# Performance work log

Hardware: AMD Instinct MI355X
Metric: run time of the kernel (lower is better)

Reference implementation:

```python
import jax, jax.numpy as jnp
import numpy as np
from jax import lax

B, K, D = 8, 256, 256
T_FRAMES = 2048
NH, HD = 4, 64          # num_heads_upsampling = 2*num_heads, head_dim = in_dim // NH
FW = FC = 8             # filter_size_w / filter_size_c
SW, SC = 16, 2          # swish_block_units


def setup_inputs() -> dict:
    key = jax.random.key(0)
    ks = jax.random.split(key, 24)
    rn = lambda i, shape, s=0.05: jax.random.normal(ks[i], shape, jnp.float32) * s
    return {
        'phs': rn(0, (B, K, D), 1.0),
        'phs_mask': jnp.ones((B, K), bool),
        'total_duration_groundtruth': jnp.full((B,), T_FRAMES, jnp.int32),
        'T': T_FRAMES,
        'Wd': rn(1, (D, 1)), 'bd': jnp.zeros((1,), jnp.float32),
        'W1': rn(2, (D, D)), 'b1': jnp.zeros((D,), jnp.float32),
        'W2': rn(3, (D, D)), 'b2': jnp.zeros((D,), jnp.float32),
        'W3': rn(4, (D, D)), 'b3': jnp.zeros((D,), jnp.float32),
        'wconv_k': rn(5, (FW, D, 3)), 'wconv_b': jnp.zeros((FW,), jnp.float32),
        'wln_g': jnp.ones((FW,), jnp.float32), 'wln_b': jnp.zeros((FW,), jnp.float32),
        'cconv_k': rn(6, (FC, D, 3)), 'cconv_b': jnp.zeros((FC,), jnp.float32),
        'cln_g': jnp.ones((FC,), jnp.float32), 'cln_b': jnp.zeros((FC,), jnp.float32),
        'sw1_W': rn(7, (FW + 2, SW)), 'sw1_b': jnp.zeros((SW,), jnp.float32),
        'sw2_W': rn(8, (SW, SW)), 'sw2_b': jnp.zeros((SW,), jnp.float32),
        'sc1_W': rn(9, (FC + 2, SC)), 'sc1_b': jnp.zeros((SC,), jnp.float32),
        'sc2_W': rn(10, (SC, SC)), 'sc2_b': jnp.zeros((SC,), jnp.float32),
        'we_W': rn(11, (SW, NH)), 'we_b': jnp.zeros((NH,), jnp.float32),
        'ce_W': rn(12, (SC, HD)), 'ce_b': jnp.zeros((HD,), jnp.float32),
    }


def _silu(x):
    return x * jax.nn.sigmoid(x)


def _conv_ln_silu(x, kern, bias, g, beta):
    # x: (b,k,D) -> Conv1d (same pad) -> LayerNorm over channel dim -> SiLU -> (b,k,F)
    y = lax.conv_general_dilated(x.transpose(0, 2, 1), kern, (1,), [(1, 1)],
                                 dimension_numbers=('NCH', 'OIH', 'NCH'))
    y = y + bias[None, :, None]
    mu = y.mean(1, keepdims=True)
    var = y.var(1, keepdims=True)
    y = (y - mu) * lax.rsqrt(var + 1e-5) * g[None, :, None] + beta[None, :, None]
    return _silu(y).transpose(0, 2, 1)


def _forward(phs, phs_mask, total_duration_groundtruth, t,
             Wd, bd, W1, b1, W2, b2, W3, b3,
             wconv_k, wconv_b, wln_g, wln_b, cconv_k, cconv_b, cln_g, cln_b,
             sw1_W, sw1_b, sw2_W, sw2_b, sc1_W, sc1_b, sc2_W, sc2_b,
             we_W, we_b, ce_W, ce_b):
    b, k, D = phs.shape
    nh, hd = NH, HD
    v_pad = ~phs_mask                                       # (b,k)
    # duration predictor (encoder substituted by identity; see notes)
    d_log = jax.nn.relu(phs @ Wd + bd)[..., 0]              # (b,k)
    d = jnp.clip(jnp.exp(d_log) - 1.0, 1e-12)
    d = jnp.where(v_pad, 0.0, d)
    d_pad = jnp.arange(t)[None, :] >= total_duration_groundtruth[:, None]  # (b,t)
    attn_mask = v_pad[:, None, :] | d_pad[:, :, None]       # (b,t,k)
    e = jnp.cumsum(d, -1)
    s = e - d
    scale = jnp.arange(1, t + 1, dtype=phs.dtype)[None, :, None]
    s_b = jnp.where(attn_mask, 0.0, scale - s[:, None, :])  # (b,t,k)
    e_b = jnp.where(attn_mask, 0.0, e[:, None, :] - scale)
    v = phs @ W1 + b1                                        # mha_project_1
    # w path: conv features broadcast over t + per-position MLP -> softmax scores
    w_convs = _conv_ln_silu(v, wconv_k, wconv_b, wln_g, wln_b)  # (b,k,FW)
    merged_w = jnp.concatenate([s_b[..., None], e_b[..., None],
                                jnp.broadcast_to(w_convs[:, None], (b, t, k, FW))], -1)
    hw = _silu(merged_w @ sw1_W + sw1_b)
    hw = _silu(hw @ sw2_W + sw2_b)                           # (b,t,k,SW)
    logits = (hw @ we_W + we_b).transpose(0, 3, 1, 2)        # (b,nh,t,k)
    logits = jnp.where(v_pad[:, None, None, :], -jnp.inf, logits)
    attn = jax.nn.softmax(logits, -1)                        # (b,nh,t,k)
    # c path
    c_convs = _conv_ln_silu(v, cconv_k, cconv_b, cln_g, cln_b)  # (b,k,FC)
    merged_c = jnp.concatenate([s_b[..., None], e_b[..., None],
                                jnp.broadcast_to(c_convs[:, None], (b, t, k, FC))], -1)
    hc = _silu(merged_c @ sc1_W + sc1_b)
    hc = _silu(hc @ sc2_W + sc2_b)                           # (b,t,k,SC)
    ein = jnp.einsum('bhtk,btkp->bhtp', attn, hc)            # (b,nh,t,SC)
    c_extra = (ein @ ce_W + ce_b).transpose(0, 2, 1, 3)      # (b,t,nh,hd)
    v4 = v.reshape(b, k, nh, hd).transpose(0, 2, 1, 3)       # (b,nh,k,hd)
    o_left = jnp.einsum('bhtk,bhkd->bhtd', attn, v4).transpose(0, 2, 1, 3)
    o_left = o_left.reshape(b, t, nh * hd) @ W2 + b2
    o_right = c_extra.reshape(b, t, nh * hd) @ W3 + b3
    out = o_left + o_right
    return out, d, attn


def reference(phs, phs_mask, total_duration_groundtruth, T,
              Wd, bd, W1, b1, W2, b2, W3, b3,
              wconv_k, wconv_b, wln_g, wln_b, cconv_k, cconv_b, cln_g, cln_b,
              sw1_W, sw1_b, sw2_W, sw2_b, sc1_W, sc1_b, sc2_W, sc2_b,
              we_W, we_b, ce_W, ce_b):
    return _forward(phs, phs_mask, total_duration_groundtruth, int(T),
                    Wd, bd, W1, b1, W2, b2, W3, b3,
                    wconv_k, wconv_b, wln_g, wln_b, cconv_k, cconv_b, cln_g, cln_b,
                    sw1_W, sw1_b, sw2_W, sw2_b, sc1_W, sc1_b, sc2_W, sc2_b,
                    we_W, we_b, ce_W, ce_b)
```

## Files before the change

### kernel.cpp

```cpp
#include <hip/hip_runtime.h>
#include <hip/hip_bf16.h>
#include <math.h>

#define BB 8
#define KK 256
#define DD 256
#define TT 2048
#define NH 4
#define HD 64
#define FW 8
#define FC 8
#define TPB 8
#define NK2 1056

#define OFF_S    0
#define OFF_E    (OFF_S + BB*KK)
#define OFF_V    (OFF_E + BB*KK)
#define OFF_WC   (OFF_V + BB*KK*DD)
#define OFF_CC   (OFF_WC + BB*KK*FW)
#define OFF_C0   (OFF_CC + BB*KK*FC)
#define OFF_W1T  (OFF_C0 + DD)
#define OFF_W2T  (OFF_W1T + DD*DD)
#define OFF_U2B  (OFF_W2T + DD*DD)
#define OFF_EINB (OFF_U2B + BB*DD*NK2/2)
#define OFF_P3   (OFF_EINB + BB*TT*32/2)

#define OUT_OUT  0
#define OUT_D    (BB*TT*DD)
#define OUT_ATTN (OUT_D + BB*KK)

typedef __attribute__((ext_vector_type(8))) short s8v;
typedef __attribute__((ext_vector_type(4))) float f4v;
typedef __attribute__((ext_vector_type(2))) _Float16 h2v;
typedef unsigned short ushort_t;

#define BC(x) __builtin_bit_cast(h2v, (unsigned int)(x))

__device__ __forceinline__ h2v pk(float a, float b) {
    return __builtin_bit_cast(h2v, __builtin_amdgcn_cvt_pkrtz(a, b));
}
__device__ __forceinline__ ushort_t f2bf(float x) {
    unsigned u = __float_as_uint(x);
    u += 0x7fffu + ((u >> 16) & 1u);
    return (ushort_t)(u >> 16);
}

#if __has_builtin(__builtin_amdgcn_fdot2)
#define FDOT2(a,b,c) __builtin_amdgcn_fdot2((a),(b),(c),false)
#else
__device__ __forceinline__ float FDOT2(h2v a, h2v b, float c) {
    return c + (float)a[0]*(float)b[0] + (float)a[1]*(float)b[1];
}
#endif

__device__ __forceinline__ float siluf(float z) {
    return z * __builtin_amdgcn_rcpf(1.0f + __expf(-z));
}

__device__ __forceinline__ float rsum64d(float x) {
    x += __int_as_float(__builtin_amdgcn_update_dpp(0, __float_as_int(x), 0x111, 0xf, 0xf, true));
    x += __int_as_float(__builtin_amdgcn_update_dpp(0, __float_as_int(x), 0x112, 0xf, 0xf, true));
    x += __int_as_float(__builtin_amdgcn_update_dpp(0, __float_as_int(x), 0x114, 0xf, 0xf, true));
    x += __int_as_float(__builtin_amdgcn_update_dpp(0, __float_as_int(x), 0x118, 0xf, 0xf, true));
    x += __int_as_float(__builtin_amdgcn_update_dpp(0, __float_as_int(x), 0x142, 0xa, 0xf, true));
    x += __int_as_float(__builtin_amdgcn_update_dpp(0, __float_as_int(x), 0x143, 0xc, 0xf, true));
    return x;
}
__device__ __forceinline__ float rmax64d(float x) {
    const int NI = 0xff800000;
    x = fmaxf(x, __int_as_float(__builtin_amdgcn_update_dpp(NI, __float_as_int(x), 0x111, 0xf, 0xf, false)));
    x = fmaxf(x, __int_as_float(__builtin_amdgcn_update_dpp(NI, __float_as_int(x), 0x112, 0xf, 0xf, false)));
    x = fmaxf(x, __int_as_float(__builtin_amdgcn_update_dpp(NI, __float_as_int(x), 0x114, 0xf, 0xf, false)));
    x = fmaxf(x, __int_as_float(__builtin_amdgcn_update_dpp(NI, __float_as_int(x), 0x118, 0xf, 0xf, false)));
    x = fmaxf(x, __int_as_float(__builtin_amdgcn_update_dpp(NI, __float_as_int(x), 0x142, 0xa, 0xf, false)));
    x = fmaxf(x, __int_as_float(__builtin_amdgcn_update_dpp(NI, __float_as_int(x), 0x143, 0xc, 0xf, false)));
    return x;
}
__device__ __forceinline__ float lane63f(float x) {
    return __int_as_float(__builtin_amdgcn_readlane(__float_as_int(x), 63));
}

__launch_bounds__(256)
__global__ void prep(const float* __restrict__ W1, const float* __restrict__ W2,
                     const float* __restrict__ phs, const float* __restrict__ Wd,
                     const float* __restrict__ bd,
                     const float* __restrict__ ceW, const float* __restrict__ ceb,
                     const float* __restrict__ W3, const float* __restrict__ b3,
                     const float* __restrict__ b2,
                     float* __restrict__ ws, float* __restrict__ dout) {
    __shared__ float tl[64][65];
    __shared__ float dbuf[KK];
    int role = blockIdx.x, tid = threadIdx.x;
    if (role < 32) {
        const float* src = (role < 16) ? W1 : W2;
        float* dst = ws + ((role < 16) ? OFF_W1T : OFF_W2T);
        int rr = role & 15;
        int r0 = (rr >> 2)*64, c0 = (rr & 3)*64;
        int rx = tid >> 4, col4 = (tid & 15)*4;
#pragma unroll
        for (int i = 0; i < 4; ++i) {
            int row = rx + i*16;
            float4 vld = *(const float4*)&src[(size_t)(r0+row)*256 + c0 + col4];
            tl[row][col4+0]=vld.x; tl[row][col4+1]=vld.y; tl[row][col4+2]=vld.z; tl[row][col4+3]=vld.w;
        }
        __syncthreads();
#pragma unroll
        for (int i = 0; i < 4; ++i) {
            int row = rx + i*16;
            float4 vst;
            vst.x = tl[col4+0][row]; vst.y = tl[col4+1][row];
            vst.z = tl[col4+2][row]; vst.w = tl[col4+3][row];
            *(float4*)&dst[(size_t)(c0+row)*256 + r0 + col4] = vst;
        }
    } else if (role < 40) {
        int b = role - 32;
        int wave = tid >> 6, lane = tid & 63;
        float4 w4 = ((const float4*)Wd)[lane];
        float bd0 = bd[0];
        for (int kk = 0; kk < 64; ++kk) {
            int k = wave*64 + kk;
            float4 p = ((const float4*)(phs + (size_t)(b*KK + k)*DD))[lane];
            float part = p.x*w4.x + p.y*w4.y + p.z*w4.z + p.w*w4.w;
            float tot = rsum64d(part);
            if (lane == 63) {
                float acc = tot + bd0;
                float dl = fmaxf(acc, 0.f);
                dbuf[k] = fmaxf(expf(dl) - 1.f, 1e-12f);
            }
        }
        __syncthreads();
        int k = tid;
        float dv = dbuf[k];
        for (int off = 1; off < KK; off <<= 1) {
            float t = (k >= off) ? dbuf[k-off] : 0.f;
            __syncthreads();
            dbuf[k] += t;
            __syncthreads();
        }
        float e = dbuf[k];
        dout[OUT_D + b*KK + k] = dv;
        ws[OFF_S + b*KK + k] = e - dv;
        ws[OFF_E + b*KK + k] = e;
    } else {
        int b = role - 40, c = tid;
        float acc[8] = {0,0,0,0,0,0,0,0};
        float c0v = b3[c] + b2[c];
#pragma unroll 4
        for (int h = 0; h < NH; ++h) {
            for (int d = 0; d < HD; ++d) {
                float w3v = W3[(size_t)(h*HD + d)*DD + c];
                acc[h*2+0] = fmaf(ceW[d],      w3v, acc[h*2+0]);
                acc[h*2+1] = fmaf(ceW[HD + d], w3v, acc[h*2+1]);
                c0v        = fmaf(ceb[d],      w3v, c0v);
            }
        }
        ushort_t* rowp = (ushort_t*)(ws + OFF_U2B) + ((size_t)b*DD + c)*NK2 + 1024;
#pragma unroll
        for (int j = 0; j < 8; ++j) rowp[j] = f2bf(acc[j]);
#pragma unroll
        for (int j = 8; j < 32; ++j) rowp[j] = 0;
        if (b == 0) ws[OFF_C0 + c] = c0v;
    }
}

__launch_bounds__(256)
__global__ void k3a(const float* __restrict__ vsrc, const float* __restrict__ wk,
                    const float* __restrict__ ck, float* __restrict__ part) {
    __shared__ float vt[KK][33];
    __shared__ float wl[32][3][8];
    int b = blockIdx.x, ch = blockIdx.y, ph = blockIdx.z;
    const float* kern = ph ? ck : wk;
    int tid = threadIdx.x, c0 = ch*32;
    for (int i = tid; i < 768; i += 256) {
        int f = i & 7;
        int cq = i >> 3; int q = cq % 3; int cc = cq / 3;
        wl[cc][q][f] = kern[(f*DD + c0 + cc)*3 + q];
    }
    {
        int cc = tid & 31, r8 = tid >> 5;
        for (int j = 0; j < 32; ++j) {
            int row = r8 + j*8;
            vt[row][cc] = vsrc[(size_t)(b*KK + row)*DD + c0 + cc];
        }
    }
    __syncthreads();
    int k = tid;
    float y[8] = {0.f,0.f,0.f,0.f,0.f,0.f,0.f,0.f};
    bool hm = (k > 0), hp = (k < KK-1);
    for (int cc = 0; cc < 32; ++cc) {
        float xm = hm ? vt[k-1][cc] : 0.f;
        float x0 = vt[k][cc];
        float xp = hp ? vt[k+1][cc] : 0.f;
        float4 a0 = *(const float4*)&wl[cc][0][0];
        float4 a1 = *(const float4*)&wl[cc][0][4];
        float4 b0 = *(const float4*)&wl[cc][1][0];
        float4 b1 = *(const float4*)&wl[cc][1][4];
        float4 c0v = *(const float4*)&wl[cc][2][0];
        float4 c1v = *(const float4*)&wl[cc][2][4];
        y[0] = fmaf(xm, a0.x, fmaf(x0, b0.x, fmaf(xp, c0v.x, y[0])));
        y[1] = fmaf(xm, a0.y, fmaf(x0, b0.y, fmaf(xp, c0v.y, y[1])));
        y[2] = fmaf(xm, a0.z, fmaf(x0, b0.z, fmaf(xp, c0v.z, y[2])));
        y[3] = fmaf(xm, a0.w, fmaf(x0, b0.w, fmaf(xp, c0v.w, y[3])));
        y[4] = fmaf(xm, a1.x, fmaf(x0, b1.x, fmaf(xp, c1v.x, y[4])));
        y[5] = fmaf(xm, a1.y, fmaf(x0, b1.y, fmaf(xp, c1v.y, y[5])));
        y[6] = fmaf(xm, a1.z, fmaf(x0, b1.z, fmaf(xp, c1v.z, y[6])));
        y[7] = fmaf(xm, a1.w, fmaf(x0, b1.w, fmaf(xp, c1v.w, y[7])));
    }
    float* pp = part + ((((size_t)(b*2 + ph))*8 + ch)*KK + k)*8;
    *(float4*)&pp[0] = make_float4(y[0],y[1],y[2],y[3]);
    *(float4*)&pp[4] = make_float4(y[4],y[5],y[6],y[7]);
}

__global__ void k3b(float* __restrict__ ws_, const float* __restrict__ part,
                    const float* __restrict__ wb, const float* __restrict__ wg, const float* __restrict__ wbe,
                    const float* __restrict__ cb, const float* __restrict__ cg, const float* __restrict__ cbe) {
    int b = blockIdx.x, k = threadIdx.x;
#pragma unroll
    for (int ph = 0; ph < 2; ++ph) {
        const float* bias = ph ? cb : wb;
        const float* g    = ph ? cg : wg;
        const float* beta = ph ? cbe : wbe;
        float y[8];
#pragma unroll
        for (int f = 0; f < 8; ++f) y[f] = bias[f];
        for (int ch = 0; ch < 8; ++ch) {
            const float* pp = part + ((((size_t)(b*2 + ph))*8 + ch)*KK + k)*8;
            float4 q0 = *(const float4*)&pp[0];
            float4 q1 = *(const float4*)&pp[4];
            y[0]+=q0.x; y[1]+=q0.y; y[2]+=q0.z; y[3]+=q0.w;
            y[4]+=q1.x; y[5]+=q1.y; y[6]+=q1.z; y[7]+=q1.w;
        }
        float mu = 0.f;
#pragma unroll
        for (int f = 0; f < 8; ++f) mu += y[f];
        mu *= 0.125f;
        float var = 0.f;
#pragma unroll
        for (int f = 0; f < 8; ++f) { float dd = y[f]-mu; var = fmaf(dd, dd, var); }
        var *= 0.125f;
        float inv = rsqrtf(var + 1e-5f);
        float* dst = ws_ + (ph ? OFF_CC : OFF_WC) + (size_t)(b*KK + k)*8;
#pragma unroll
        for (int f = 0; f < 8; ++f) {
            float z = (y[f]-mu)*inv*g[f] + beta[f];
            dst[f] = siluf(z);
        }
    }
}

__launch_bounds__(256, 3)
__global__ void k4_main(const float* __restrict__ ws, const int* __restrict__ tdur,
                        const float* __restrict__ sw1W, const float* __restrict__ sw1b,
                        const float* __restrict__ sw2W, const float* __restrict__ sw2b,
                        const float* __restrict__ weW, const float* __restrict__ web,
                        const float* __restrict__ sc1W, const float* __restrict__ sc1b,
                        const float* __restrict__ sc2W, const float* __restrict__ sc2b,
                        float* __restrict__ dout, ushort_t* __restrict__ einb) {
    __shared__ float sw1s[160];
    __shared__ float sw1bs[16];
    __shared__ float sc1s[20];
    __shared__ float sc1bs[2];
    __shared__ h2v   sw2h[16][8];
    __shared__ float sw2bias[16];
    __shared__ float wes4[16][4];
    __shared__ float webs[4], sc2s[4], sc2bs[2];
    __shared__ float red[4][4][16];
    __shared__ float gbuf[4][4][4];
    int tid = threadIdx.x;
    int b = blockIdx.y;
    int t0 = blockIdx.x * TPB;
    int lane = tid & 63, wid = tid >> 6;

    if (tid < 160) sw1s[tid] = sw1W[tid];
    if (tid < 16)  { sw1bs[tid] = sw1b[tid]; sw2bias[tid] = sw2b[tid]; }
    if (tid < 20)  sc1s[tid] = sc1W[tid];
    if (tid < 2)   { sc1bs[tid] = sc1b[tid]; sc2bs[tid] = sc2b[tid]; }
    if (tid < 4)   { webs[tid] = web[tid]; sc2s[tid] = sc2W[tid]; }
    if (tid < 128) {
        int j = tid >> 3, ip = tid & 7;
        sw2h[j][ip] = pk(sw2W[(2*ip)*16 + j], sw2W[(2*ip+1)*16 + j]);
    }
    if (tid < 64) wes4[tid>>2][tid&3] = weW[tid];
    __syncthreads();

    int k = tid;
    float s_k = ws[OFF_S + b*KK + k];
    float e_k = ws[OFF_E + b*KK + k];
    float al[16], be[16];
    float lgm[4], p2m[2];
    {
        float wcf[8];
        const float* wp = ws + OFF_WC + (size_t)(b*KK + k)*8;
#pragma unroll
        for (int f = 0; f < 8; ++f) wcf[f] = wp[f];
        float bw[16];
#pragma unroll
        for (int j = 0; j < 16; ++j) {
            float z = sw1bs[j];
#pragma unroll
            for (int f = 0; f < 8; ++f) z = fmaf(wcf[f], sw1s[(2+f)*16 + j], z);
            bw[j] = z;
        }
        h2v h1pm[8];
#pragma unroll
        for (int ip = 0; ip < 8; ++ip)
            h1pm[ip] = pk(siluf(bw[2*ip]), siluf(bw[2*ip+1]));
        lgm[0]=webs[0]; lgm[1]=webs[1]; lgm[2]=webs[2]; lgm[3]=webs[3];
#pragma unroll
        for (int j = 0; j < 16; ++j) {
            const uint4* wpq = (const uint4*)&sw2h[j][0];
            uint4 wa = wpq[0], wb = wpq[1];
            float z = sw2bias[j];
            z = FDOT2(h1pm[0], BC(wa.x), z); z = FDOT2(h1pm[1], BC(wa.y), z);
            z = FDOT2(h1pm[2], BC(wa.z), z); z = FDOT2(h1pm[3], BC(wa.w), z);
            z = FDOT2(h1pm[4], BC(wb.x), z); z = FDOT2(h1pm[5], BC(wb.y), z);
            z = FDOT2(h1pm[6], BC(wb.z), z); z = FDOT2(h1pm[7], BC(wb.w), z);
            float g = siluf(z);
            float4 wv = *(const float4*)&wes4[j][0];
            lgm[0] = fmaf(g, wv.x, lgm[0]); lgm[1] = fmaf(g, wv.y, lgm[1]);
            lgm[2] = fmaf(g, wv.z, lgm[2]); lgm[3] = fmaf(g, wv.w, lgm[3]);
        }
#pragma unroll
        for (int j = 0; j < 16; ++j) {
            float wsj = sw1s[j], wej = sw1s[16 + j];
            be[j] = wsj - wej;
            al[j] = bw[j] - wsj*s_k + wej*e_k;
        }
    }
    float gc[2], dc[2];
    {
        float ccf[8];
        const float* cp = ws + OFF_CC + (size_t)(b*KK + k)*8;
#pragma unroll
        for (int f = 0; f < 8; ++f) ccf[f] = cp[f];
        float bc0 = sc1bs[0], bc1 = sc1bs[1];
#pragma unroll
        for (int f = 0; f < 8; ++f) {
            bc0 = fmaf(ccf[f], sc1s[(2+f)*2 + 0], bc0);
            bc1 = fmaf(ccf[f], sc1s[(2+f)*2 + 1], bc1);
        }
        gc[0] = sc1s[0] - sc1s[2]; gc[1] = sc1s[1] - sc1s[3];
        dc[0] = bc0 - sc1s[0]*s_k + sc1s[2]*e_k;
        dc[1] = bc1 - sc1s[1]*s_k + sc1s[3]*e_k;
        float p1m0 = siluf(bc0), p1m1 = siluf(bc1);
        p2m[0] = siluf(p1m0*sc2s[0] + p1m1*sc2s[2] + sc2bs[0]);
        p2m[1] = siluf(p1m0*sc2s[1] + p1m1*sc2s[3] + sc2bs[1]);
    }
    float sc2r0 = sc2s[0], sc2r1 = sc2s[1], sc2r2 = sc2s[2], sc2r3 = sc2s[3];
    float sc2b0 = sc2bs[0], sc2b1 = sc2bs[1];
    float web0 = webs[0], web1 = webs[1], web2 = webs[2], web3 = webs[3];
    int td = tdur[b];

    for (int tg = 0; tg < TPB; tg += 4) {
        int tbase = t0 + tg;
        h2v h1p[4][8];
        float p2v[4][2];
        float lg[4][4];
        float ex[4][4];
#pragma unroll
        for (int u = 0; u < 4; ++u) {
            float tp1 = (float)(tbase + u + 1);
#pragma unroll
            for (int ip = 0; ip < 8; ++ip) {
                float z0 = siluf(fmaf(tp1, be[2*ip], al[2*ip]));
                float z1 = siluf(fmaf(tp1, be[2*ip+1], al[2*ip+1]));
                h1p[u][ip] = pk(z0, z1);
            }
            float p10 = siluf(fmaf(tp1, gc[0], dc[0]));
            float p11 = siluf(fmaf(tp1, gc[1], dc[1]));
            p2v[u][0] = siluf(p10*sc2r0 + p11*sc2r2 + sc2b0);
            p2v[u][1] = siluf(p10*sc2r1 + p11*sc2r3 + sc2b1);
            lg[u][0]=web0; lg[u][1]=web1; lg[u][2]=web2; lg[u][3]=web3;
        }
#pragma unroll
        for (int j = 0; j < 16; ++j) {
            const uint4* wpq = (const uint4*)&sw2h[j][0];
            uint4 wa = wpq[0], wb = wpq[1];
            h2v w0=BC(wa.x), w1=BC(wa.y), w2=BC(wa.z), w3=BC(wa.w);
            h2v w4_=BC(wb.x), w5=BC(wb.y), w6=BC(wb.z), w7=BC(wb.w);
            float bias = sw2bias[j];
            float4 wv = *(const float4*)&wes4[j][0];
#pragma unroll
            for (int u = 0; u < 4; ++u) {
                float z = bias;
                z = FDOT2(h1p[u][0], w0, z); z = FDOT2(h1p[u][1], w1, z);
                z = FDOT2(h1p[u][2], w2, z); z = FDOT2(h1p[u][3], w3, z);
                z = FDOT2(h1p[u][4], w4_, z); z = FDOT2(h1p[u][5], w5, z);
                z = FDOT2(h1p[u][6], w6, z); z = FDOT2(h1p[u][7], w7, z);
                float g = siluf(z);
                lg[u][0] = fmaf(g, wv.x, lg[u][0]);
                lg[u][1] = fmaf(g, wv.y, lg[u][1]);
                lg[u][2] = fmaf(g, wv.z, lg[u][2]);
                lg[u][3] = fmaf(g, wv.w, lg[u][3]);
            }
        }
#pragma unroll
        for (int u = 0; u < 4; ++u) {
            if ((tbase + u) >= td) {
                lg[u][0]=lgm[0]; lg[u][1]=lgm[1]; lg[u][2]=lgm[2]; lg[u][3]=lgm[3];
                p2v[u][0]=p2m[0]; p2v[u][1]=p2m[1];
            }
        }
#pragma unroll
        for (int u = 0; u < 4; ++u) {
            float m0 = lane63f(rmax64d(lg[u][0]));
            float m1 = lane63f(rmax64d(lg[u][1]));
            float m2 = lane63f(rmax64d(lg[u][2]));
            float m3 = lane63f(rmax64d(lg[u][3]));
            ex[u][0] = __expf(lg[u][0] - m0);
            ex[u][1] = __expf(lg[u][1] - m1);
            ex[u][2] = __expf(lg[u][2] - m2);
            ex[u][3] = __expf(lg[u][3] - m3);
            float s0 = rsum64d(ex[u][0]), s1 = rsum64d(ex[u][1]);
            float s2 = rsum64d(ex[u][2]), s3 = rsum64d(ex[u][3]);
            float u0 = rsum64d(ex[u][0]*p2v[u][0]);
            float u1 = rsum64d(ex[u][0]*p2v[u][1]);
            float u2 = rsum64d(ex[u][1]*p2v[u][0]);
            float u3 = rsum64d(ex[u][1]*p2v[u][1]);
            float u4 = rsum64d(ex[u][2]*p2v[u][0]);
            float u5 = rsum64d(ex[u][2]*p2v[u][1]);
            float u6 = rsum64d(ex[u][3]*p2v[u][0]);
            float u7 = rsum64d(ex[u][3]*p2v[u][1]);
            if (lane == 63) {
                float* rr = &red[u][wid][0];
                *(float4*)&rr[0]  = make_float4(m0, m1, m2, m3);
                *(float4*)&rr[4]  = make_float4(s0, s1, s2, s3);
                *(float4*)&rr[8]  = make_float4(u0, u1, u2, u3);
                *(float4*)&rr[12] = make_float4(u4, u5, u6, u7);
            }
        }
        __syncthreads();
        if (tid < 64) {
            int u = tid >> 4, h = (tid >> 2) & 3, w = tid & 3;
            float m0 = red[u][0][h], m1 = red[u][1][h], m2 = red[u][2][h], m3 = red[u][3][h];
            float M = fmaxf(fmaxf(m0, m1), fmaxf(m2, m3));
            float f0 = __expf(m0 - M), f1 = __expf(m1 - M);
            float f2 = __expf(m2 - M), f3 = __expf(m3 - M);
            float S = red[u][0][4+h]*f0 + red[u][1][4+h]*f1
                    + red[u][2][4+h]*f2 + red[u][3][4+h]*f3;
            float fw = (w == 0) ? f0 : ((w == 1) ? f1 : ((w == 2) ? f2 : f3));
            gbuf[u][w][h] = fw * __builtin_amdgcn_rcpf(S);
        } else if (tid < 96) {
            int idx = tid - 64, u = idx >> 3, j = idx & 7, h = j >> 1;
            float m0 = red[u][0][h], m1 = red[u][1][h], m2 = red[u][2][h], m3 = red[u][3][h];
            float M = fmaxf(fmaxf(m0, m1), fmaxf(m2, m3));
            float f0 = __expf(m0 - M), f1 = __expf(m1 - M);
            float f2 = __expf(m2 - M), f3 = __expf(m3 - M);
            float S = red[u][0][4+h]*f0 + red[u][1][4+h]*f1
                    + red[u][2][4+h]*f2 + red[u][3][4+h]*f3;
            float num = red[u][0][8+j]*f0 + red[u][1][8+j]*f1
                      + red[u][2][8+j]*f2 + red[u][3][8+j]*f3;
            einb[((size_t)b*TT + tbase + u)*32 + j] = f2bf(num * __builtin_amdgcn_rcpf(S));
        } else if (tid < 192) {
            int idx = tid - 96, u = idx / 24, r = idx - u*24;
            einb[((size_t)b*TT + tbase + u)*32 + 8 + r] = 0;
        }
        __syncthreads();
#pragma unroll
        for (int u = 0; u < 4; ++u) {
            int t = tbase + u;
            float4 g4 = *(const float4*)&gbuf[u][wid][0];
            dout[OUT_ATTN + ((size_t)(b*NH + 0)*TT + t)*KK + k] = ex[u][0] * g4.x;
            dout[OUT_ATTN + ((size_t)(b*NH + 1)*TT + t)*KK + k] = ex[u][1] * g4.y;
            dout[OUT_ATTN + ((size_t)(b*NH + 2)*TT + t)*KK + k] = ex[u][2] * g4.z;
            dout[OUT_ATTN + ((size_t)(b*NH + 3)*TT + t)*KK + k] = ex[u][3] * g4.w;
        }
    }
}

#define MLDA 56
__launch_bounds__(256, 2)
__global__ void kmm(const float* __restrict__ A, const float* __restrict__ B,
                    float* __restrict__ C, const float* __restrict__ bias,
                    int Kd, int lda, int ldb, int ldc) {
    int m0 = blockIdx.x * 128, n0 = blockIdx.y * 128;
    __shared__ ushort_t Asl[128*MLDA];
    __shared__ ushort_t Bsl[128*MLDA];
    int tid = threadIdx.x;
    int lane = tid & 63, wid = tid >> 6;
    int wm = wid & 1, wn = wid >> 1;
    int quad = lane >> 4, lo = lane & 15;
    f4v acc[4][4];
#pragma unroll
    for (int i = 0; i < 4; ++i)
#pragma unroll
        for (int j = 0; j < 4; ++j) { f4v zz = {0.f,0.f,0.f,0.f}; acc[i][j] = zz; }
    int srow = tid >> 3;
    int scol = (tid & 7) * 4;
    for (int k0 = 0; k0 < Kd; k0 += 32) {
#pragma unroll
        for (int i = 0; i < 4; ++i) {
            int r = srow + i*32;
            float4 va = *(const float4*)&A[(size_t)(m0 + r)*lda + k0 + scol];
            float4 vb = *(const float4*)&B[(size_t)(n0 + r)*ldb + k0 + scol];
            __hip_bfloat162 pa0 = __float22bfloat162_rn(make_float2(va.x, va.y));
            __hip_bfloat162 pa1 = __float22bfloat162_rn(make_float2(va.z, va.w));
            __hip_bfloat162 pb0 = __float22bfloat162_rn(make_float2(vb.x, vb.y));
            __hip_bfloat162 pb1 = __float22bfloat162_rn(make_float2(vb.z, vb.w));
            *(uint2*)&Asl[r*MLDA + scol] = make_uint2(*(unsigned int*)&pa0, *(unsigned int*)&pa1);
            *(uint2*)&Bsl[r*MLDA + scol] = make_uint2(*(unsigned int*)&pb0, *(unsigned int*)&pb1);
        }
        __syncthreads();
        s8v af[4], bf[4];
#pragma unroll
        for (int mt = 0; mt < 4; ++mt)
            af[mt] = *(const s8v*)&Asl[(wm*64 + mt*16 + lo)*MLDA + quad*8];
#pragma unroll
        for (int nt = 0; nt < 4; ++nt)
            bf[nt] = *(const s8v*)&Bsl[(wn*64 + nt*16 + lo)*MLDA + quad*8];
#pragma unroll
        for (int mt = 0; mt < 4; ++mt)
#pragma unroll
            for (int nt = 0; nt < 4; ++nt)
                acc[mt][nt] = __builtin_amdgcn_mfma_f32_16x16x32_bf16(af[mt], bf[nt], acc[mt][nt], 0, 0, 0);
        __syncthreads();
    }
#pragma unroll
    for (int mt = 0; mt < 4; ++mt)
#pragma unroll
        for (int nt = 0; nt < 4; ++nt) {
            int col = n0 + wn*64 + nt*16 + lo;
            float bv = bias ? bias[col] : 0.f;
#pragma unroll
            for (int r = 0; r < 4; ++r) {
                int row = m0 + wm*64 + mt*16 + quad*4 + r;
                C[(size_t)row*ldc + col] = acc[mt][nt][r] + bv;
            }
        }
}

__launch_bounds__(256, 2)
__global__ void kmmB(const float* __restrict__ A, const float* __restrict__ B,
                     ushort_t* __restrict__ C,
                     int Kd, int lda, int ldb, int ldc,
                     long sA2, long sB1, long sB2, long sC1, long sC2, int nz2) {
    int z = blockIdx.z, z1 = z / nz2, z2 = z - z1*nz2;
    A += (size_t)z2*sA2;
    B += (size_t)z1*sB1 + (size_t)z2*sB2;
    C += (size_t)z1*sC1 + (size_t)z2*sC2;
    int m0 = blockIdx.x * 128, n0 = blockIdx.y * 128;
    __shared__ ushort_t Asl[128*MLDA];
    __shared__ ushort_t Bsl[128*MLDA];
    int tid = threadIdx.x;
    int lane = tid & 63, wid = tid >> 6;
    int wm = wid & 1, wn = wid >> 1;
    int quad = lane >> 4, lo = lane & 15;
    f4v acc[4][4];
#pragma unroll
    for (int i = 0; i < 4; ++i)
#pragma unroll
        for (int j = 0; j < 4; ++j) { f4v zz = {0.f,0.f,0.f,0.f}; acc[i][j] = zz; }
    int srow = tid >> 3;
    int scol = (tid & 7) * 4;
    for (int k0 = 0; k0 < Kd; k0 += 32) {
#pragma unroll
        for (int i = 0; i < 4; ++i) {
            int r = srow + i*32;
            float4 va = *(const float4*)&A[(size_t)(m0 + r)*lda + k0 + scol];
            float4 vb = *(const float4*)&B[(size_t)(n0 + r)*ldb + k0 + scol];
            __hip_bfloat162 pa0 = __float22bfloat162_rn(make_float2(va.x, va.y));
            __hip_bfloat162 pa1 = __float22bfloat162_rn(make_float2(va.z, va.w));
            __hip_bfloat162 pb0 = __float22bfloat162_rn(make_float2(vb.x, vb.y));
            __hip_bfloat162 pb1 = __float22bfloat162_rn(make_float2(vb.z, vb.w));
            *(uint2*)&Asl[r*MLDA + scol] = make_uint2(*(unsigned int*)&pa0, *(unsigned int*)&pa1);
            *(uint2*)&Bsl[r*MLDA + scol] = make_uint2(*(unsigned int*)&pb0, *(unsigned int*)&pb1);
        }
        __syncthreads();
        s8v af[4], bf[4];
#pragma unroll
        for (int mt = 0; mt < 4; ++mt)
            af[mt] = *(const s8v*)&Asl[(wm*64 + mt*16 + lo)*MLDA + quad*8];
#pragma unroll
        for (int nt = 0; nt < 4; ++nt)
            bf[nt] = *(const s8v*)&Bsl[(wn*64 + nt*16 + lo)*MLDA + quad*8];
#pragma unroll
        for (int mt = 0; mt < 4; ++mt)
#pragma unroll
            for (int nt = 0; nt < 4; ++nt)
                acc[mt][nt] = __builtin_amdgcn_mfma_f32_16x16x32_bf16(af[mt], bf[nt], acc[mt][nt], 0, 0, 0);
        __syncthreads();
    }
#pragma unroll
    for (int mt = 0; mt < 4; ++mt)
#pragma unroll
        for (int nt = 0; nt < 4; ++nt) {
            int col = n0 + wn*64 + nt*16 + lo;
#pragma unroll
            for (int r = 0; r < 4; ++r) {
                int row = m0 + wm*64 + mt*16 + quad*4 + r;
                C[(size_t)row*ldc + col] = f2bf(acc[mt][nt][r]);
            }
        }
}

__launch_bounds__(256, 2)
__global__ void kOL2(const float* __restrict__ attn, const ushort_t* __restrict__ einb,
                     const ushort_t* __restrict__ U2B, const float* __restrict__ C0,
                     float* __restrict__ out) {
    __shared__ ushort_t Asl[128*MLDA];
    __shared__ ushort_t Bsl[128*MLDA];
    int b = blockIdx.z;
    int t0 = blockIdx.x * 128, c0 = blockIdx.y * 128;
    int tid = threadIdx.x;
    int lane = tid & 63, wid = tid >> 6;
    int wm = wid & 1, wn = wid >> 1;
    int quad = lane >> 4, lo = lane & 15;
    f4v acc[4][4];
#pragma unroll
    for (int i = 0; i < 4; ++i)
#pragma unroll
        for (int j = 0; j < 4; ++j) { f4v zz = {0.f,0.f,0.f,0.f}; acc[i][j] = zz; }
    const float* Ab = attn + (size_t)b*NH*TT*KK;
    const ushort_t* Bb = U2B + (size_t)b*DD*NK2;
    int srow = tid >> 3;
    int scol = (tid & 7) * 4;
    int rB = tid >> 2;
    int cB = (tid & 3) * 8;
    for (int k0 = 0; k0 < NK2; k0 += 32) {
        if (k0 < NH*KK) {
            const float* ag = Ab + ((size_t)((k0 >> 8)*TT + t0))*KK + (k0 & 255);
#pragma unroll
            for (int i = 0; i < 4; ++i) {
                int r = srow + i*32;
                float4 va = *(const float4*)(ag + (size_t)r*KK + scol);
                __hip_bfloat162 pa0 = __float22bfloat162_rn(make_float2(va.x, va.y));
                __hip_bfloat162 pa1 = __float22bfloat162_rn(make_float2(va.z, va.w));
                *(uint2*)&Asl[r*MLDA + scol] = make_uint2(*(unsigned int*)&pa0, *(unsigned int*)&pa1);
            }
        } else {
            const ushort_t* ag = einb + ((size_t)b*TT + t0)*32;
#pragma unroll
            for (int i = 0; i < 2; ++i) {
                int r = rB + i*64;
                uint4 w = *(const uint4*)(ag + (size_t)r*32 + cB);
                *(uint4*)&Asl[r*MLDA + cB] = w;
            }
        }
        {
            const ushort_t* bg = Bb + (size_t)c0*NK2 + k0;
#pragma unroll
            for (int i = 0; i < 2; ++i) {
                int r = rB + i*64;
                uint4 w = *(const uint4*)(bg + (size_t)r*NK2 + cB);
                *(uint4*)&Bsl[r*MLDA + cB] = w;
            }
        }
        __syncthreads();
        s8v af[4], bf[4];
#pragma unroll
        for (int mt = 0; mt < 4; ++mt)
            af[mt] = *(const s8v*)&Asl[(wm*64 + mt*16 + lo)*MLDA + quad*8];
#pragma unroll
        for (int nt = 0; nt < 4; ++nt)
            bf[nt] = *(const s8v*)&Bsl[(wn*64 + nt*16 + lo)*MLDA + quad*8];
#pragma unroll
        for (int mt = 0; mt < 4; ++mt)
#pragma unroll
            for (int nt = 0; nt < 4; ++nt)
                acc[mt][nt] = __builtin_amdgcn_mfma_f32_16x16x32_bf16(af[mt], bf[nt], acc[mt][nt], 0, 0, 0);
        __syncthreads();
    }
#pragma unroll
    for (int mt = 0; mt < 4; ++mt)
#pragma unroll
        for (int nt = 0; nt < 4; ++nt) {
            int col = c0 + wn*64 + nt*16 + lo;
            float bv = C0[col];
#pragma unroll
            for (int r = 0; r < 4; ++r) {
                int row = t0 + wm*64 + mt*16 + quad*4 + r;
                out[((size_t)b*TT + row)*DD + col] = acc[mt][nt][r] + bv;
            }
        }
}

extern "C" void kernel_launch(void* const* d_in, const int* in_sizes, int n_in,
                              void* d_out, int out_size, void* d_ws, size_t ws_size,
                              hipStream_t stream) {
    const float* phs  = (const float*)d_in[0];
    const int*   tdur = (const int*)d_in[2];
    const float* Wd   = (const float*)d_in[4];
    const float* bd   = (const float*)d_in[5];
    const float* W1   = (const float*)d_in[6];
    const float* b1   = (const float*)d_in[7];
    const float* W2   = (const float*)d_in[8];
    const float* b2   = (const float*)d_in[9];
    const float* W3   = (const float*)d_in[10];
    const float* b3   = (const float*)d_in[11];
    const float* wck  = (const float*)d_in[12];
    const float* wcb  = (const float*)d_in[13];
    const float* wlg  = (const float*)d_in[14];
    const float* wlb  = (const float*)d_in[15];
    const float* cck  = (const float*)d_in[16];
    const float* ccb  = (const float*)d_in[17];
    const float* clg  = (const float*)d_in[18];
    const float* clb  = (const float*)d_in[19];
    const float* sw1W = (const float*)d_in[20];
    const float* sw1b = (const float*)d_in[21];
    const float* sw2W = (const float*)d_in[22];
    const float* sw2b = (const float*)d_in[23];
    const float* sc1W = (const float*)d_in[24];
    const float* sc1b = (const float*)d_in[25];
    const float* sc2W = (const float*)d_in[26];
    const float* sc2b = (const float*)d_in[27];
    const float* weW  = (const float*)d_in[28];
    const float* web  = (const float*)d_in[29];
    const float* ceW  = (const float*)d_in[30];
    const float* ceb  = (const float*)d_in[31];

    float* out = (float*)d_out;
    float* ws  = (float*)d_ws;
    ushort_t* U2B  = (ushort_t*)(ws + OFF_U2B);
    ushort_t* EINB = (ushort_t*)(ws + OFF_EINB);

    prep<<<48, 256, 0, stream>>>(W1, W2, phs, Wd, bd, ceW, ceb, W3, b3, b2, ws, out);
    kmm<<<dim3(16,2,1), 256, 0, stream>>>(phs, ws + OFF_W1T, ws + OFF_V, b1,
        256, 256, 256, 256);
    k3a<<<dim3(BB,8,2), 256, 0, stream>>>(ws + OFF_V, wck, cck, ws + OFF_P3);
    k3b<<<BB, 256, 0, stream>>>(ws, ws + OFF_P3, wcb, wlg, wlb, ccb, clg, clb);
    kmmB<<<dim3(2,2,32), 256, 0, stream>>>(ws + OFF_W2T, ws + OFF_V, U2B,
        64, 256, 256, NK2,
        64, (long)KK*DD, 64, (long)DD*NK2, 256, 4);
    k4_main<<<dim3(TT/TPB, BB), 256, 0, stream>>>(ws, tdur, sw1W, sw1b, sw2W, sw2b,
                                                  weW, web, sc1W, sc1b, sc2W, sc2b,
                                                  out, EINB);
    kOL2<<<dim3(TT/128, 2, BB), 256, 0, stream>>>(out + OUT_ATTN, EINB, U2B,
                                                  ws + OFF_C0, out);
}
```

Measured before the change: 376.0 us.

## Retile output GEMM to 64x128 with K-step 64 and pre-zeroed einb padding

The final attention-times-U2 GEMM now uses 64-row tiles with a K step of 64 (two MFMA k-slices per stage) instead of 128-row tiles with a K step of 32. This doubles the grid and targets 4 blocks per CU, and halves the number of barrier-separated iterations. The padded K extent grows to 1088, and the zero padding of einb moves from k4_main into extra prep blocks. The trade-off is more redundant B-tile loads per output and more zero-padded MFMA work.

```diff
diff --git a/kernel.cpp b/kernel.cpp
--- a/kernel.cpp
+++ b/kernel.cpp
@@ -11,7 +11,7 @@
 #define FW 8
 #define FC 8
 #define TPB 8
-#define NK2 1056
+#define NK3 1088
 
 #define OFF_S    0
 #define OFF_E    (OFF_S + BB*KK)
@@ -22,8 +22,8 @@
 #define OFF_W1T  (OFF_C0 + DD)
 #define OFF_W2T  (OFF_W1T + DD*DD)
 #define OFF_U2B  (OFF_W2T + DD*DD)
-#define OFF_EINB (OFF_U2B + BB*DD*NK2/2)
-#define OFF_P3   (OFF_EINB + BB*TT*32/2)
+#define OFF_EINB (OFF_U2B + BB*DD*NK3/2)
+#define OFF_P3   (OFF_EINB + BB*TT*64/2)
 
 #define OUT_OUT  0
 #define OUT_D    (BB*TT*DD)
@@ -141,7 +141,7 @@
         dout[OUT_D + b*KK + k] = dv;
         ws[OFF_S + b*KK + k] = e - dv;
         ws[OFF_E + b*KK + k] = e;
-    } else {
+    } else if (role < 48) {
         int b = role - 40, c = tid;
         float acc[8] = {0,0,0,0,0,0,0,0};
         float c0v = b3[c] + b2[c];
@@ -154,12 +154,20 @@
                 c0v        = fmaf(ceb[d],      w3v, c0v);
             }
         }
-        ushort_t* rowp = (ushort_t*)(ws + OFF_U2B) + ((size_t)b*DD + c)*NK2 + 1024;
+        ushort_t* rowp = (ushort_t*)(ws + OFF_U2B) + ((size_t)b*DD + c)*NK3 + 1024;
 #pragma unroll
         for (int j = 0; j < 8; ++j) rowp[j] = f2bf(acc[j]);
 #pragma unroll
-        for (int j = 8; j < 32; ++j) rowp[j] = 0;
+        for (int j = 8; j < 64; ++j) rowp[j] = 0;
         if (b == 0) ws[OFF_C0 + c] = c0v;
+    } else {
+        uint4* ez = (uint4*)((ushort_t*)(ws + OFF_EINB));
+        int base = (role - 48) * 2048 + tid;
+#pragma unroll
+        for (int i = 0; i < 8; ++i) {
+            uint4 z; z.x = 0; z.y = 0; z.z = 0; z.w = 0;
+            ez[base + i*256] = z;
+        }
     }
 }
 
@@ -450,10 +458,7 @@
                     + red[u][2][4+h]*f2 + red[u][3][4+h]*f3;
             float num = red[u][0][8+j]*f0 + red[u][1][8+j]*f1
                       + red[u][2][8+j]*f2 + red[u][3][8+j]*f3;
-            einb[((size_t)b*TT + tbase + u)*32 + j] = f2bf(num * __builtin_amdgcn_rcpf(S));
-        } else if (tid < 192) {
-            int idx = tid - 96, u = idx / 24, r = idx - u*24;
-            einb[((size_t)b*TT + tbase + u)*32 + 8 + r] = 0;
+            einb[((size_t)b*TT + tbase + u)*64 + j] = f2bf(num * __builtin_amdgcn_rcpf(S));
         }
         __syncthreads();
 #pragma unroll
@@ -593,82 +598,80 @@
         }
 }
 
-__launch_bounds__(256, 2)
-__global__ void kOL2(const float* __restrict__ attn, const ushort_t* __restrict__ einb,
+#define OLD 72
+__launch_bounds__(256, 4)
+__global__ void kOL3(const float* __restrict__ attn, const ushort_t* __restrict__ einb,
                      const ushort_t* __restrict__ U2B, const float* __restrict__ C0,
                      float* __restrict__ out) {
-    __shared__ ushort_t Asl[128*MLDA];
-    __shared__ ushort_t Bsl[128*MLDA];
+    __shared__ ushort_t Asl[64*OLD];
+    __shared__ ushort_t Bsl[128*OLD];
     int b = blockIdx.z;
-    int t0 = blockIdx.x * 128, c0 = blockIdx.y * 128;
+    int t0 = blockIdx.x * 64, c0 = blockIdx.y * 128;
     int tid = threadIdx.x;
     int lane = tid & 63, wid = tid >> 6;
     int wm = wid & 1, wn = wid >> 1;
     int quad = lane >> 4, lo = lane & 15;
-    f4v acc[4][4];
-#pragma unroll
-    for (int i = 0; i < 4; ++i)
+    f4v acc[2][4];
+#pragma unroll
+    for (int i = 0; i < 2; ++i)
 #pragma unroll
         for (int j = 0; j < 4; ++j) { f4v zz = {0.f,0.f,0.f,0.f}; acc[i][j] = zz; }
     const float* Ab = attn + (size_t)b*NH*TT*KK;
-    const ushort_t* Bb = U2B + (size_t)b*DD*NK2;
-    int srow = tid >> 3;
-    int scol = (tid & 7) * 4;
-    int rB = tid >> 2;
-    int cB = (tid & 3) * 8;
-    for (int k0 = 0; k0 < NK2; k0 += 32) {
+    const ushort_t* Bb = U2B + (size_t)b*DD*NK3;
+    int rA = tid >> 2, cA = (tid & 3) * 16;
+    int rB = tid >> 1, cB = (tid & 1) * 32;
+    for (int k0 = 0; k0 < NK3; k0 += 64) {
         if (k0 < NH*KK) {
-            const float* ag = Ab + ((size_t)((k0 >> 8)*TT + t0))*KK + (k0 & 255);
+            const float* ag = Ab + ((size_t)((k0 >> 8)*TT + t0 + rA))*KK + (k0 & 255) + cA;
 #pragma unroll
             for (int i = 0; i < 4; ++i) {
-                int r = srow + i*32;
-                float4 va = *(const float4*)(ag + (size_t)r*KK + scol);
-                __hip_bfloat162 pa0 = __float22bfloat162_rn(make_float2(va.x, va.y));
-                __hip_bfloat162 pa1 = __float22bfloat162_rn(make_float2(va.z, va.w));
-                *(uint2*)&Asl[r*MLDA + scol] = make_uint2(*(unsigned int*)&pa0, *(unsigned int*)&pa1);
+                float4 va = *(const float4*)(ag + i*4);
+                __hip_bfloat162 p0 = __float22bfloat162_rn(make_float2(va.x, va.y));
+                __hip_bfloat162 p1 = __float22bfloat162_rn(make_float2(va.z, va.w));
+                *(uint2*)&Asl[rA*OLD + cA + i*4] = make_uint2(*(unsigned int*)&p0, *(unsigned int*)&p1);
             }
         } else {
-            const ushort_t* ag = einb + ((size_t)b*TT + t0)*32;
-#pragma unroll
-            for (int i = 0; i < 2; ++i) {
-                int r = rB + i*64;
-                uint4 w = *(const uint4*)(ag + (size_t)r*32 + cB);
-                *(uint4*)&Asl[r*MLDA + cB] = w;
-            }
+            const ushort_t* ag = einb + ((size_t)b*TT + t0 + rA)*64 + cA;
+#pragma unroll
+            for (int i = 0; i < 2; ++i)
+                *(uint4*)&Asl[rA*OLD + cA + i*8] = *(const uint4*)(ag + i*8);
         }
         {
-            const ushort_t* bg = Bb + (size_t)c0*NK2 + k0;
-#pragma unroll
-            for (int i = 0; i < 2; ++i) {
-                int r = rB + i*64;
-                uint4 w = *(const uint4*)(bg + (size_t)r*NK2 + cB);
-                *(uint4*)&Bsl[r*MLDA + cB] = w;
-            }
-        }
-        __syncthreads();
-        s8v af[4], bf[4];
-#pragma unroll
-        for (int mt = 0; mt < 4; ++mt)
-            af[mt] = *(const s8v*)&Asl[(wm*64 + mt*16 + lo)*MLDA + quad*8];
+            const ushort_t* bg = Bb + (size_t)(c0 + rB)*NK3 + k0 + cB;
+#pragma unroll
+            for (int i = 0; i < 4; ++i)
+                *(uint4*)&Bsl[rB*OLD + cB + i*8] = *(const uint4*)(bg + i*8);
+        }
+        __syncthreads();
+        s8v af[2][2], bf[4][2];
+#pragma unroll
+        for (int mt = 0; mt < 2; ++mt)
+#pragma unroll
+            for (int ks = 0; ks < 2; ++ks)
+                af[mt][ks] = *(const s8v*)&Asl[(wm*32 + mt*16 + lo)*OLD + ks*32 + quad*8];
 #pragma unroll
         for (int nt = 0; nt < 4; ++nt)
-            bf[nt] = *(const s8v*)&Bsl[(wn*64 + nt*16 + lo)*MLDA + quad*8];
-#pragma unroll
-        for (int mt = 0; mt < 4; ++mt)
+#pragma unroll
+            for (int ks = 0; ks < 2; ++ks)
+                bf[nt][ks] = *(const s8v*)&Bsl[(wn*64 + nt*16 + lo)*OLD + ks*32 + quad*8];
+#pragma unroll
+        for (int mt = 0; mt < 2; ++mt)
 #pragma unroll
             for (int nt = 0; nt < 4; ++nt)
-                acc[mt][nt] = __builtin_amdgcn_mfma_f32_16x16x32_bf16(af[mt], bf[nt], acc[mt][nt], 0, 0, 0);
-        __syncthreads();
-    }
-#pragma unroll
-    for (int mt = 0; mt < 4; ++mt)
+#pragma unroll
+                for (int ks = 0; ks < 2; ++ks)
+                    acc[mt][nt] = __builtin_amdgcn_mfma_f32_16x16x32_bf16(af[mt][ks], bf[nt][ks], acc[mt][nt], 0, 0, 0);
+        __syncthreads();
+    }
+#pragma unroll
+    for (int mt = 0; mt < 2; ++mt)
 #pragma unroll
         for (int nt = 0; nt < 4; ++nt) {
             int col = c0 + wn*64 + nt*16 + lo;
             float bv = C0[col];
 #pragma unroll
             for (int r = 0; r < 4; ++r) {
-                int row = t0 + wm*64 + mt*16 + quad*4 + r;
+                int row = t0 + wm*32 + mt*16 + quad*4 + r;
                 out[((size_t)b*TT + row)*DD + col] = acc[mt][nt][r] + bv;
             }
         }
@@ -713,17 +716,17 @@
     ushort_t* U2B  = (ushort_t*)(ws + OFF_U2B);
     ushort_t* EINB = (ushort_t*)(ws + OFF_EINB);
 
-    prep<<<48, 256, 0, stream>>>(W1, W2, phs, Wd, bd, ceW, ceb, W3, b3, b2, ws, out);
+    prep<<<112, 256, 0, stream>>>(W1, W2, phs, Wd, bd, ceW, ceb, W3, b3, b2, ws, out);
     kmm<<<dim3(16,2,1), 256, 0, stream>>>(phs, ws + OFF_W1T, ws + OFF_V, b1,
         256, 256, 256, 256);
     k3a<<<dim3(BB,8,2), 256, 0, stream>>>(ws + OFF_V, wck, cck, ws + OFF_P3);
     k3b<<<BB, 256, 0, stream>>>(ws, ws + OFF_P3, wcb, wlg, wlb, ccb, clg, clb);
     kmmB<<<dim3(2,2,32), 256, 0, stream>>>(ws + OFF_W2T, ws + OFF_V, U2B,
-        64, 256, 256, NK2,
-        64, (long)KK*DD, 64, (long)DD*NK2, 256, 4);
+        64, 256, 256, NK3,
+        64, (long)KK*DD, 64, (long)DD*NK3, 256, 4);
     k4_main<<<dim3(TT/TPB, BB), 256, 0, stream>>>(ws, tdur, sw1W, sw1b, sw2W, sw2b,
                                                   weW, web, sc1W, sc1b, sc2W, sc2b,
                                                   out, EINB);
-    kOL2<<<dim3(TT/128, 2, BB), 256, 0, stream>>>(out + OUT_ATTN, EINB, U2B,
-                                                  ws + OFF_C0, out);
-}
+    kOL3<<<dim3(TT/64, 2, BB), 256, 0, stream>>>(out + OUT_ATTN, EINB, U2B,
+                                                 ws + OFF_C0, out);
+}
```

New measurement: 366.6 us. -2.5%, faster.
